# Optimization experiments

Measured on AMD Instinct MI355X. Metric: run time of the kernel, lower is better.

## Reference

```python
import jax, jax.numpy as jnp
import numpy as np

T, B, F, L = 512, 4096, 16, 4  # seq_len, batch, input_size, n_layers; hidden_size H = 1


def _lstm_layer(seq, W_ih, W_hh, b_ih, b_hh):
    """Single unidirectional LSTM layer, H=1.
    seq: [T, B, in]; W_ih: [4, in]; W_hh: [4, 1]; b_ih, b_hh: [4].
    Returns (hs [T,B,1], h_T [B,1], c_T [B,1]). Gate order i,f,g,o (PyTorch).
    """
    # Input contribution for all timesteps at once (the only sizeable GEMM).
    gx = jnp.einsum('tbi,gi->tbg', seq, W_ih) + b_ih + b_hh  # [T, B, 4]
    Bb = seq.shape[1]
    h0 = jnp.zeros((Bb, 1), seq.dtype)
    c0 = jnp.zeros((Bb, 1), seq.dtype)

    def step(carry, g):
        h, c = carry
        gates = g + h @ W_hh.T  # [B, 4]
        i = jax.nn.sigmoid(gates[:, 0:1])
        f = jax.nn.sigmoid(gates[:, 1:2])
        gg = jnp.tanh(gates[:, 2:3])
        o = jax.nn.sigmoid(gates[:, 3:4])
        c = f * c + i * gg
        h = o * jnp.tanh(c)
        return (h, c), h

    (hT, cT), hs = jax.lax.scan(step, (h0, c0), gx)
    return hs, hT, cT


def setup_inputs() -> dict:
    key = jax.random.key(0)
    ks = jax.random.split(key, 6)
    s = 0.5  # ~U(-1,1) stdev scale; 1/sqrt(H)=1 in torch init
    return {
        'x': jax.random.normal(ks[0], (T, B, F), jnp.float32),
        'W_ih0': jax.random.normal(ks[1], (4, F), jnp.float32) * s,
        'W_ih_rest': jax.random.normal(ks[2], (L - 1, 4, 1), jnp.float32) * s,
        'W_hh': jax.random.normal(ks[3], (L, 4, 1), jnp.float32) * s,
        'b_ih': jax.random.normal(ks[4], (L, 4), jnp.float32) * s,
        'b_hh': jax.random.normal(ks[5], (L, 4), jnp.float32) * s,
    }


def reference(x, W_ih0, W_ih_rest, W_hh, b_ih, b_hh):
    seq = x
    hns, cns = [], []
    for l in range(L):
        W_ih_l = W_ih0 if l == 0 else W_ih_rest[l - 1]
        seq, hT, cT = _lstm_layer(seq, W_ih_l, W_hh[l], b_ih[l], b_hh[l])
        hns.append(hT)
        cns.append(cT)
    output = seq                      # [T, B, 1] last-layer hidden sequence
    hn = jnp.stack(hns, axis=0)       # [L, B, 1]
    cn = jnp.stack(cns, axis=0)       # [L, B, 1]
    return output, hn, cn
```

## Files before the change

### kernel.cpp

```cpp
#include <hip/hip_runtime.h>

#define T_DIM 512
#define B_DIM 4096
#define F_DIM 16
#define L_DIM 4

typedef float f4 __attribute__((ext_vector_type(4)));

__device__ __forceinline__ float fast_sigmoid(float x) {
  return __builtin_amdgcn_rcpf(1.0f + __builtin_amdgcn_exp2f(-1.44269504089f * x));
}
__device__ __forceinline__ float fast_tanh(float x) {
  return 1.0f - 2.0f * __builtin_amdgcn_rcpf(1.0f + __builtin_amdgcn_exp2f(2.88539008178f * x));
}

__device__ __forceinline__ float dpp_prev(float v) {
  int r = __builtin_amdgcn_update_dpp(0, __builtin_bit_cast(int, v),
                                      0x111 , 0xf, 0xf, true);
  return __builtin_bit_cast(float, r);
}
template <int CTRL>
__device__ __forceinline__ float dpp_qp(float v) {
  int r = __builtin_amdgcn_update_dpp(0, __builtin_bit_cast(int, v),
                                      CTRL, 0xf, 0xf, true);
  return __builtin_bit_cast(float, r);
}

__device__ __forceinline__ void ld_f4(f4& dst, unsigned voff, const f4* base) {
  asm volatile("global_load_dwordx4 %0, %1, %2"
               : "=v"(dst) : "v"(voff), "s"(base) : "memory");
}
__device__ __forceinline__ void wait_ring(f4* buf) {
  asm volatile("s_waitcnt vmcnt(0)"
               : "+v"(buf[0]), "+v"(buf[1]), "+v"(buf[2]), "+v"(buf[3]),
                 "+v"(buf[4]), "+v"(buf[5]), "+v"(buf[6]), "+v"(buf[7])
               :: "memory");
}

__global__ __launch_bounds__(256) void gx0_kernel(
    const f4* __restrict__ x4, const f4* __restrict__ W4,
    const float* __restrict__ bih, const float* __restrict__ bhh,
    float* __restrict__ gx) {
  const int gidx = blockIdx.x * 256 + threadIdx.x;
  const int q = gidx & 3;
  f4 xv = x4[gidx];
  float p[4];
#pragma unroll
  for (int g = 0; g < 4; ++g) {
    f4 wv = W4[g * 4 + q];
    p[g] = fmaf(xv.x, wv.x, fmaf(xv.y, wv.y, fmaf(xv.z, wv.z, xv.w * wv.w)));
  }
#pragma unroll
  for (int g = 0; g < 4; ++g) {
    p[g] += dpp_qp<0xB1>(p[g]);
    p[g] += dpp_qp<0x4E>(p[g]);
  }
  float r = (q == 0) ? p[0] : (q == 1) ? p[1] : (q == 2) ? p[2] : p[3];
  gx[gidx] = r + bih[q] + bhh[q];
}

__global__ __launch_bounds__(64, 1) void lstm_scan_skew(
    const f4* __restrict__ gx,
    const float* __restrict__ Wrest,
    const float* __restrict__ Whh,
    const float* __restrict__ bih, const float* __restrict__ bhh,
    float* __restrict__ out) {
  const int lane = threadIdx.x;
  const int l = lane & 3;
  const int b = blockIdx.x * 16 + (lane >> 2);
  const bool l0 = (l == 0);
  const float gsel = l0 ? 1.0f : 0.0f;

  float wih[4], whh[4], base[4];
#pragma unroll
  for (int g = 0; g < 4; ++g) {
    whh[g]  = Whh[l * 4 + g];
    wih[g]  = l0 ? 0.0f : Wrest[(l - 1) * 4 + g];
    base[g] = l0 ? 0.0f : (bih[l * 4 + g] + bhh[l * 4 + g]);
  }

  float* __restrict__ po = out + b;
  float h = 0.f, c = 0.f;

  unsigned vj[8];
#pragma unroll
  for (int j = 0; j < 8; ++j) vj[j] = (unsigned)b * 16u + (unsigned)j * 65536u;

  f4 A[8], B[8];

  auto cell = [&](int k, f4 gq, bool guard) {
    float hin = dpp_prev(h);
    float g0 = fmaf(whh[0], h, fmaf(wih[0], hin, fmaf(gsel, gq.x, base[0])));
    float g1 = fmaf(whh[1], h, fmaf(wih[1], hin, fmaf(gsel, gq.y, base[1])));
    float g2 = fmaf(whh[2], h, fmaf(wih[2], hin, fmaf(gsel, gq.z, base[2])));
    float g3 = fmaf(whh[3], h, fmaf(wih[3], hin, fmaf(gsel, gq.w, base[3])));
    float i_ = fast_sigmoid(g0);
    float f_ = fast_sigmoid(g1);
    float gg = fast_tanh(g2);
    float o_ = fast_sigmoid(g3);
    float cn = fmaf(f_, c, i_ * gg);
    float hn = o_ * fast_tanh(cn);
    if (guard) {
      const int t = k - l;
      const bool valid = (unsigned)t < (unsigned)T_DIM;
      c = valid ? cn : c;
      h = valid ? hn : h;
      if (l == 3 && valid) po[(size_t)t * B_DIM] = hn;
    } else {
      c = cn; h = hn;
      if (l == 3) po[(size_t)(k - 3) * B_DIM] = hn;
    }
  };
  auto cells8 = [&](int k0, f4* buf, bool guard) {
#pragma unroll
    for (int j = 0; j < 8; ++j) cell(k0 + j, buf[j], guard);
  };
  auto load8 = [&](f4* buf, int tbase) {
    const f4* p = gx + (size_t)tbase * B_DIM;
#pragma unroll
    for (int j = 0; j < 8; ++j) ld_f4(buf[j], vj[j], p);
  };

  load8(A, 0);
  wait_ring(A);
  load8(B, 8);
  cells8(0, A, true);

#pragma unroll 1
  for (int n = 1; n < 63; n += 2) {
    wait_ring(B);
    load8(A, 8 * (n + 1));
    cells8(8 * n, B, false);
    wait_ring(A);
    load8(B, 8 * (n + 2));
    cells8(8 * (n + 1), A, false);
  }
  wait_ring(B);
  load8(A, 504);
  cells8(504, B, false);
  wait_ring(A);
  cells8(512, A, true);

  po[(size_t)T_DIM * B_DIM + (size_t)l * B_DIM] = h;
  po[(size_t)T_DIM * B_DIM + (size_t)L_DIM * B_DIM + (size_t)l * B_DIM] = c;
}

__global__ __launch_bounds__(64) void lstm_scan_fused(
    const float* __restrict__ x, const float* __restrict__ Wih0,
    const float* __restrict__ Wrest, const float* __restrict__ Whh,
    const float* __restrict__ bih, const float* __restrict__ bhh,
    float* __restrict__ out) {
  const int b = blockIdx.x * 64 + threadIdx.x;
  float whh_[4][4];
#pragma unroll
  for (int l = 0; l < 4; ++l)
#pragma unroll
    for (int g = 0; g < 4; ++g) whh_[l][g] = Whh[l * 4 + g];
  float wih_[3][4], base_[3][4];
#pragma unroll
  for (int l = 0; l < 3; ++l)
#pragma unroll
    for (int g = 0; g < 4; ++g) {
      wih_[l][g]  = Wrest[l * 4 + g];
      base_[l][g] = bih[(l + 1) * 4 + g] + bhh[(l + 1) * 4 + g];
    }
  float base0[4], wih0r[4][16];
#pragma unroll
  for (int g = 0; g < 4; ++g) {
    base0[g] = bih[g] + bhh[g];
#pragma unroll
    for (int i = 0; i < 16; ++i) wih0r[g][i] = Wih0[g * 16 + i];
  }
  float h[4] = {0.f,0.f,0.f,0.f}, c[4] = {0.f,0.f,0.f,0.f};
  for (int t = 0; t < T_DIM; ++t) {
    const float4* xr = (const float4*)x + ((size_t)t * B_DIM + b) * 4;
    float xs[16];
    *(float4*)&xs[0] = xr[0]; *(float4*)&xs[4] = xr[1];
    *(float4*)&xs[8] = xr[2]; *(float4*)&xs[12] = xr[3];
    float a0 = base0[0], a1 = base0[1], a2 = base0[2], a3 = base0[3];
#pragma unroll
    for (int i = 0; i < 16; ++i) {
      a0 = fmaf(wih0r[0][i], xs[i], a0);
      a1 = fmaf(wih0r[1][i], xs[i], a1);
      a2 = fmaf(wih0r[2][i], xs[i], a2);
      a3 = fmaf(wih0r[3][i], xs[i], a3);
    }
    float i_ = fast_sigmoid(fmaf(whh_[0][0], h[0], a0));
    float f_ = fast_sigmoid(fmaf(whh_[0][1], h[0], a1));
    float gg = fast_tanh(fmaf(whh_[0][2], h[0], a2));
    float o_ = fast_sigmoid(fmaf(whh_[0][3], h[0], a3));
    c[0] = fmaf(f_, c[0], i_ * gg);
    h[0] = o_ * fast_tanh(c[0]);
#pragma unroll
    for (int l = 1; l < 4; ++l) {
      float hin = h[l - 1];
      float gi = fmaf(whh_[l][0], h[l], fmaf(wih_[l-1][0], hin, base_[l-1][0]));
      float gf = fmaf(whh_[l][1], h[l], fmaf(wih_[l-1][1], hin, base_[l-1][1]));
      float gG = fmaf(whh_[l][2], h[l], fmaf(wih_[l-1][2], hin, base_[l-1][2]));
      float go = fmaf(whh_[l][3], h[l], fmaf(wih_[l-1][3], hin, base_[l-1][3]));
      float ii = fast_sigmoid(gi), ff = fast_sigmoid(gf);
      float gg2 = fast_tanh(gG), oo = fast_sigmoid(go);
      c[l] = fmaf(ff, c[l], ii * gg2);
      h[l] = oo * fast_tanh(c[l]);
    }
    out[(size_t)t * B_DIM + b] = h[3];
  }
#pragma unroll
  for (int l = 0; l < 4; ++l) {
    out[(size_t)T_DIM * B_DIM + (size_t)l * B_DIM + b] = h[l];
    out[(size_t)T_DIM * B_DIM + (size_t)L_DIM * B_DIM + (size_t)l * B_DIM + b] = c[l];
  }
}

extern "C" void kernel_launch(void* const* d_in, const int* in_sizes, int n_in,
                              void* d_out, int out_size, void* d_ws, size_t ws_size,
                              hipStream_t stream) {
  const float* x     = (const float*)d_in[0];
  const float* Wih0  = (const float*)d_in[1];
  const float* Wrest = (const float*)d_in[2];
  const float* Whh   = (const float*)d_in[3];
  const float* bih   = (const float*)d_in[4];
  const float* bhh   = (const float*)d_in[5];
  float* out = (float*)d_out;

  const size_t gx_bytes = (size_t)T_DIM * B_DIM * 4 * sizeof(float);
  if (ws_size >= gx_bytes) {
    float* gx = (float*)d_ws;
    const int nquarters = T_DIM * B_DIM * 4;
    gx0_kernel<<<nquarters / 256, 256, 0, stream>>>(
        (const f4*)x, (const f4*)Wih0, bih, bhh, gx);
    lstm_scan_skew<<<B_DIM / 16, 64, 0, stream>>>(
        (const f4*)gx, Wrest, Whh, bih, bhh, out);
  } else {
    lstm_scan_fused<<<B_DIM / 64, 64, 0, stream>>>(x, Wih0, Wrest, Whh, bih, bhh, out);
  }
}
```

Measured before the change: 261.6 us.

## Fuse layer-0 input projection into skewed scan kernel and fold gate scaling

```diff
diff --git a/kernel.cpp b/kernel.cpp
--- a/kernel.cpp
+++ b/kernel.cpp
@@ -2,17 +2,10 @@
 
 #define T_DIM 512
 #define B_DIM 4096
-#define F_DIM 16
 #define L_DIM 4
+#define LOG2E 1.44269504088896f
 
 typedef float f4 __attribute__((ext_vector_type(4)));
-
-__device__ __forceinline__ float fast_sigmoid(float x) {
-  return __builtin_amdgcn_rcpf(1.0f + __builtin_amdgcn_exp2f(-1.44269504089f * x));
-}
-__device__ __forceinline__ float fast_tanh(float x) {
-  return 1.0f - 2.0f * __builtin_amdgcn_rcpf(1.0f + __builtin_amdgcn_exp2f(2.88539008178f * x));
-}
 
 __device__ __forceinline__ float dpp_prev(float v) {
   int r = __builtin_amdgcn_update_dpp(0, __builtin_bit_cast(int, v),
@@ -20,10 +13,10 @@
   return __builtin_bit_cast(float, r);
 }
 template <int CTRL>
-__device__ __forceinline__ float dpp_qp(float v) {
+__device__ __forceinline__ float qp_add(float v) {
   int r = __builtin_amdgcn_update_dpp(0, __builtin_bit_cast(int, v),
                                       CTRL, 0xf, 0xf, true);
-  return __builtin_bit_cast(float, r);
+  return v + __builtin_bit_cast(float, r);
 }
 
 __device__ __forceinline__ void ld_f4(f4& dst, unsigned voff, const f4* base) {
@@ -37,30 +30,9 @@
                :: "memory");
 }
 
-__global__ __launch_bounds__(256) void gx0_kernel(
-    const f4* __restrict__ x4, const f4* __restrict__ W4,
-    const float* __restrict__ bih, const float* __restrict__ bhh,
-    float* __restrict__ gx) {
-  const int gidx = blockIdx.x * 256 + threadIdx.x;
-  const int q = gidx & 3;
-  f4 xv = x4[gidx];
-  float p[4];
-#pragma unroll
-  for (int g = 0; g < 4; ++g) {
-    f4 wv = W4[g * 4 + q];
-    p[g] = fmaf(xv.x, wv.x, fmaf(xv.y, wv.y, fmaf(xv.z, wv.z, xv.w * wv.w)));
-  }
-#pragma unroll
-  for (int g = 0; g < 4; ++g) {
-    p[g] += dpp_qp<0xB1>(p[g]);
-    p[g] += dpp_qp<0x4E>(p[g]);
-  }
-  float r = (q == 0) ? p[0] : (q == 1) ? p[1] : (q == 2) ? p[2] : p[3];
-  gx[gidx] = r + bih[q] + bhh[q];
-}
-
-__global__ __launch_bounds__(64, 1) void lstm_scan_skew(
-    const f4* __restrict__ gx,
+__global__ __launch_bounds__(64, 1) void lstm_fused(
+    const float* __restrict__ x,
+    const float* __restrict__ Wih0,
     const float* __restrict__ Wrest,
     const float* __restrict__ Whh,
     const float* __restrict__ bih, const float* __restrict__ bhh,
@@ -71,145 +43,114 @@
   const bool l0 = (l == 0);
   const float gsel = l0 ? 1.0f : 0.0f;
 
+  const float sg[4] = {-LOG2E, -LOG2E, 2.0f * LOG2E, -LOG2E};
+
   float wih[4], whh[4], base[4];
+  f4 w4[4];
 #pragma unroll
   for (int g = 0; g < 4; ++g) {
-    whh[g]  = Whh[l * 4 + g];
-    wih[g]  = l0 ? 0.0f : Wrest[(l - 1) * 4 + g];
-    base[g] = l0 ? 0.0f : (bih[l * 4 + g] + bhh[l * 4 + g]);
+    whh[g]  = sg[g] * Whh[l * 4 + g];
+    wih[g]  = l0 ? 0.0f : sg[g] * Wrest[(l - 1) * 4 + g];
+    base[g] = sg[g] * (bih[l * 4 + g] + bhh[l * 4 + g]);
+    f4 wv = ((const f4*)Wih0)[g * 4 + l];
+    w4[g].x = sg[g] * wv.x; w4[g].y = sg[g] * wv.y;
+    w4[g].z = sg[g] * wv.z; w4[g].w = sg[g] * wv.w;
   }
 
   float* __restrict__ po = out + b;
   float h = 0.f, c = 0.f;
+  float hsv[8];
 
+  const char* xb = (const char*)x + (size_t)blockIdx.x * 1024;
   unsigned vj[8];
 #pragma unroll
-  for (int j = 0; j < 8; ++j) vj[j] = (unsigned)b * 16u + (unsigned)j * 65536u;
+  for (int j = 0; j < 8; ++j) vj[j] = (unsigned)lane * 16u + (unsigned)j * 262144u;
 
-  f4 A[8], B[8];
+  f4 A[8], Bq[8];
 
-  auto cell = [&](int k, f4 gq, bool guard) {
+  auto load8 = [&](f4* buf, int t0) {
+    const f4* p = (const f4*)(xb + (size_t)t0 * 262144);
+#pragma unroll
+    for (int j = 0; j < 8; ++j) ld_f4(buf[j], vj[j], p);
+  };
+
+  auto cell = [&](int k, int j, f4 xv, bool guard) {
+    float p0 = fmaf(xv.w, w4[0].w, fmaf(xv.z, w4[0].z, fmaf(xv.y, w4[0].y, xv.x * w4[0].x)));
+    float p1 = fmaf(xv.w, w4[1].w, fmaf(xv.z, w4[1].z, fmaf(xv.y, w4[1].y, xv.x * w4[1].x)));
+    float p2 = fmaf(xv.w, w4[2].w, fmaf(xv.z, w4[2].z, fmaf(xv.y, w4[2].y, xv.x * w4[2].x)));
+    float p3 = fmaf(xv.w, w4[3].w, fmaf(xv.z, w4[3].z, fmaf(xv.y, w4[3].y, xv.x * w4[3].x)));
+    p0 = qp_add<0x4E>(qp_add<0xB1>(p0));
+    p1 = qp_add<0x4E>(qp_add<0xB1>(p1));
+    p2 = qp_add<0x4E>(qp_add<0xB1>(p2));
+    p3 = qp_add<0x4E>(qp_add<0xB1>(p3));
+
     float hin = dpp_prev(h);
-    float g0 = fmaf(whh[0], h, fmaf(wih[0], hin, fmaf(gsel, gq.x, base[0])));
-    float g1 = fmaf(whh[1], h, fmaf(wih[1], hin, fmaf(gsel, gq.y, base[1])));
-    float g2 = fmaf(whh[2], h, fmaf(wih[2], hin, fmaf(gsel, gq.z, base[2])));
-    float g3 = fmaf(whh[3], h, fmaf(wih[3], hin, fmaf(gsel, gq.w, base[3])));
-    float i_ = fast_sigmoid(g0);
-    float f_ = fast_sigmoid(g1);
-    float gg = fast_tanh(g2);
-    float o_ = fast_sigmoid(g3);
-    float cn = fmaf(f_, c, i_ * gg);
-    float hn = o_ * fast_tanh(cn);
+
+    float g0 = fmaf(whh[0], h, fmaf(wih[0], hin, fmaf(gsel, p0, base[0])));
+    float g1 = fmaf(whh[1], h, fmaf(wih[1], hin, fmaf(gsel, p1, base[1])));
+    float g2 = fmaf(whh[2], h, fmaf(wih[2], hin, fmaf(gsel, p2, base[2])));
+    float g3 = fmaf(whh[3], h, fmaf(wih[3], hin, fmaf(gsel, p3, base[3])));
+
+    float Ad = 1.0f + __builtin_amdgcn_exp2f(g0);
+    float Bd = 1.0f + __builtin_amdgcn_exp2f(g1);
+    float Cd = 1.0f + __builtin_amdgcn_exp2f(g2);
+    float Dd = 1.0f + __builtin_amdgcn_exp2f(g3);
+    float rAB = __builtin_amdgcn_rcpf(Ad * Bd);
+    float rCD = __builtin_amdgcn_rcpf(Cd * Dd);
+    float i_ = rAB * Bd;
+    float f_ = rAB * Ad;
+    float tg = fmaf(-2.0f, rCD * Dd, 1.0f);
+    float o_ = rCD * Cd;
+
+    float cn  = fmaf(f_, c, i_ * tg);
+    float ecn = __builtin_amdgcn_exp2f(2.88539008178f * cn);
+    float tcn = fmaf(-2.0f, __builtin_amdgcn_rcpf(1.0f + ecn), 1.0f);
+    float hn  = o_ * tcn;
+
     if (guard) {
       const int t = k - l;
       const bool valid = (unsigned)t < (unsigned)T_DIM;
       c = valid ? cn : c;
       h = valid ? hn : h;
-      if (l == 3 && valid) po[(size_t)t * B_DIM] = hn;
     } else {
       c = cn; h = hn;
-      if (l == 3) po[(size_t)(k - 3) * B_DIM] = hn;
     }
+    hsv[j] = hn;
   };
   auto cells8 = [&](int k0, f4* buf, bool guard) {
 #pragma unroll
-    for (int j = 0; j < 8; ++j) cell(k0 + j, buf[j], guard);
+    for (int j = 0; j < 8; ++j) cell(k0 + j, j, buf[j], guard);
   };
-  auto load8 = [&](f4* buf, int tbase) {
-    const f4* p = gx + (size_t)tbase * B_DIM;
+  auto flush = [&](int k0, int jlo, int jhi) {
+    if (l == 3) {
 #pragma unroll
-    for (int j = 0; j < 8; ++j) ld_f4(buf[j], vj[j], p);
+      for (int j = 0; j < 8; ++j)
+        if (j >= jlo && j <= jhi)
+          po[(size_t)(k0 + j - 3) * B_DIM] = hsv[j];
+    }
   };
 
   load8(A, 0);
   wait_ring(A);
-  load8(B, 8);
+  load8(Bq, 8);
   cells8(0, A, true);
-
+  wait_ring(Bq); flush(0, 3, 7);  load8(A, 16);  cells8(8, Bq, false);
+  wait_ring(A);  flush(8, 0, 7);  load8(Bq, 24); cells8(16, A, false);
 #pragma unroll 1
-  for (int n = 1; n < 63; n += 2) {
-    wait_ring(B);
-    load8(A, 8 * (n + 1));
-    cells8(8 * n, B, false);
-    wait_ring(A);
-    load8(B, 8 * (n + 2));
+  for (int n = 3; n < 63; n += 2) {
+    wait_ring(Bq); flush(8 * (n - 1), 0, 7); load8(A, 8 * (n + 1));
+    cells8(8 * n, Bq, false);
+    wait_ring(A);  flush(8 * n, 0, 7);       load8(Bq, 8 * (n + 2));
     cells8(8 * (n + 1), A, false);
   }
-  wait_ring(B);
-  load8(A, 504);
-  cells8(504, B, false);
-  wait_ring(A);
-  cells8(512, A, true);
+  wait_ring(Bq); flush(8 * 62, 0, 7);
+  cells8(504, Bq, false);
+  flush(504, 0, 7);
+  cells8(512, Bq, true);
+  flush(512, 0, 2);
 
   po[(size_t)T_DIM * B_DIM + (size_t)l * B_DIM] = h;
   po[(size_t)T_DIM * B_DIM + (size_t)L_DIM * B_DIM + (size_t)l * B_DIM] = c;
-}
-
-__global__ __launch_bounds__(64) void lstm_scan_fused(
-    const float* __restrict__ x, const float* __restrict__ Wih0,
-    const float* __restrict__ Wrest, const float* __restrict__ Whh,
-    const float* __restrict__ bih, const float* __restrict__ bhh,
-    float* __restrict__ out) {
-  const int b = blockIdx.x * 64 + threadIdx.x;
-  float whh_[4][4];
-#pragma unroll
-  for (int l = 0; l < 4; ++l)
-#pragma unroll
-    for (int g = 0; g < 4; ++g) whh_[l][g] = Whh[l * 4 + g];
-  float wih_[3][4], base_[3][4];
-#pragma unroll
-  for (int l = 0; l < 3; ++l)
-#pragma unroll
-    for (int g = 0; g < 4; ++g) {
-      wih_[l][g]  = Wrest[l * 4 + g];
-      base_[l][g] = bih[(l + 1) * 4 + g] + bhh[(l + 1) * 4 + g];
-    }
-  float base0[4], wih0r[4][16];
-#pragma unroll
-  for (int g = 0; g < 4; ++g) {
-    base0[g] = bih[g] + bhh[g];
-#pragma unroll
-    for (int i = 0; i < 16; ++i) wih0r[g][i] = Wih0[g * 16 + i];
-  }
-  float h[4] = {0.f,0.f,0.f,0.f}, c[4] = {0.f,0.f,0.f,0.f};
-  for (int t = 0; t < T_DIM; ++t) {
-    const float4* xr = (const float4*)x + ((size_t)t * B_DIM + b) * 4;
-    float xs[16];
-    *(float4*)&xs[0] = xr[0]; *(float4*)&xs[4] = xr[1];
-    *(float4*)&xs[8] = xr[2]; *(float4*)&xs[12] = xr[3];
-    float a0 = base0[0], a1 = base0[1], a2 = base0[2], a3 = base0[3];
-#pragma unroll
-    for (int i = 0; i < 16; ++i) {
-      a0 = fmaf(wih0r[0][i], xs[i], a0);
-      a1 = fmaf(wih0r[1][i], xs[i], a1);
-      a2 = fmaf(wih0r[2][i], xs[i], a2);
-      a3 = fmaf(wih0r[3][i], xs[i], a3);
-    }
-    float i_ = fast_sigmoid(fmaf(whh_[0][0], h[0], a0));
-    float f_ = fast_sigmoid(fmaf(whh_[0][1], h[0], a1));
-    float gg = fast_tanh(fmaf(whh_[0][2], h[0], a2));
-    float o_ = fast_sigmoid(fmaf(whh_[0][3], h[0], a3));
-    c[0] = fmaf(f_, c[0], i_ * gg);
-    h[0] = o_ * fast_tanh(c[0]);
-#pragma unroll
-    for (int l = 1; l < 4; ++l) {
-      float hin = h[l - 1];
-      float gi = fmaf(whh_[l][0], h[l], fmaf(wih_[l-1][0], hin, base_[l-1][0]));
-      float gf = fmaf(whh_[l][1], h[l], fmaf(wih_[l-1][1], hin, base_[l-1][1]));
-      float gG = fmaf(whh_[l][2], h[l], fmaf(wih_[l-1][2], hin, base_[l-1][2]));
-      float go = fmaf(whh_[l][3], h[l], fmaf(wih_[l-1][3], hin, base_[l-1][3]));
-      float ii = fast_sigmoid(gi), ff = fast_sigmoid(gf);
-      float gg2 = fast_tanh(gG), oo = fast_sigmoid(go);
-      c[l] = fmaf(ff, c[l], ii * gg2);
-      h[l] = oo * fast_tanh(c[l]);
-    }
-    out[(size_t)t * B_DIM + b] = h[3];
-  }
-#pragma unroll
-  for (int l = 0; l < 4; ++l) {
-    out[(size_t)T_DIM * B_DIM + (size_t)l * B_DIM + b] = h[l];
-    out[(size_t)T_DIM * B_DIM + (size_t)L_DIM * B_DIM + (size_t)l * B_DIM + b] = c[l];
-  }
 }
 
 extern "C" void kernel_launch(void* const* d_in, const int* in_sizes, int n_in,
@@ -222,16 +163,5 @@
   const float* bih   = (const float*)d_in[4];
   const float* bhh   = (const float*)d_in[5];
   float* out = (float*)d_out;
-
-  const size_t gx_bytes = (size_t)T_DIM * B_DIM * 4 * sizeof(float);
-  if (ws_size >= gx_bytes) {
-    float* gx = (float*)d_ws;
-    const int nquarters = T_DIM * B_DIM * 4;
-    gx0_kernel<<<nquarters / 256, 256, 0, stream>>>(
-        (const f4*)x, (const f4*)Wih0, bih, bhh, gx);
-    lstm_scan_skew<<<B_DIM / 16, 64, 0, stream>>>(
-        (const f4*)gx, Wrest, Whh, bih, bhh, out);
-  } else {
-    lstm_scan_fused<<<B_DIM / 64, 64, 0, stream>>>(x, Wih0, Wrest, Whh, bih, bhh, out);
-  }
+  lstm_fused<<<B_DIM / 16, 64, 0, stream>>>(x, Wih0, Wrest, Whh, bih, bhh, out);
 }
```

Result: no change. 262.0 us (+0.2%).
